# Kernel tuning notes

Hardware: AMD Instinct MI355X
Metric: run time of the kernel (lower is better)

Reference implementation:

```python
import jax, jax.numpy as jnp
import numpy as np

NUM_REGIONS = 20
EMBED_DIM = 768
PATCH = (4, 16, 16)          # (pd, ph, pw)
IMG = (64, 512, 512)         # (D, H, W)
B = 2
N_PATCHES = 16384


def setup_inputs() -> dict:
    key = jax.random.key(0)
    k1, k2, k3 = jax.random.split(key, 3)
    segmentation_mask = jax.random.randint(
        k1, (B, 1) + IMG, 0, NUM_REGIONS + 1, dtype=jnp.int32)
    patch_coords = jax.random.uniform(k2, (B, N_PATCHES, 3), dtype=jnp.float32)
    region_prototypes = 0.02 * jax.random.normal(
        k3, (NUM_REGIONS, EMBED_DIM), dtype=jnp.float32)
    return {"segmentation_mask": segmentation_mask,
            "patch_coords": patch_coords,
            "region_prototypes": region_prototypes}


def _compute_assignments(segmentation_mask, patch_coords):
    Bsz, _, D, H, W = segmentation_mask.shape
    pd, ph, pw = PATCH
    dims = jnp.array([D, H, W], dtype=jnp.float32)
    half = jnp.array([pd // 2, ph // 2, pw // 2], dtype=jnp.float32)

    cpix = patch_coords * dims                                   # (B,N,3)
    # torch: z_start = max(0, int(c - half)); z_end = min(D, int(c + half))
    start = jnp.maximum(0.0, jnp.floor(cpix - half)).astype(jnp.int32)   # (B,N,3)
    end = jnp.minimum(dims, jnp.floor(cpix + half)).astype(jnp.int32)    # (B,N,3)

    # per-axis index grids of fixed size, validity mask honors clipped box
    zi = start[..., 0:1] + jnp.arange(pd, dtype=jnp.int32)        # (B,N,pd)
    yi = start[..., 1:2] + jnp.arange(ph, dtype=jnp.int32)        # (B,N,ph)
    xi = start[..., 2:3] + jnp.arange(pw, dtype=jnp.int32)        # (B,N,pw)
    vz = zi < end[..., 0:1]
    vy = yi < end[..., 1:2]
    vx = xi < end[..., 2:3]

    ziC = jnp.clip(zi, 0, D - 1)
    yiC = jnp.clip(yi, 0, H - 1)
    xiC = jnp.clip(xi, 0, W - 1)

    # flattened gather: (B, N, pd, ph, pw) voxel values
    lin = (ziC[:, :, :, None, None] * (H * W)
           + yiC[:, :, None, :, None] * W
           + xiC[:, :, None, None, :])
    flat = segmentation_mask.reshape(Bsz, D * H * W)
    vals = jnp.take_along_axis(flat, lin.reshape(Bsz, -1), axis=1)
    vals = vals.reshape(Bsz, lin.shape[1], pd, ph, pw)
    valid = (vz[:, :, :, None, None]
             & vy[:, :, None, :, None]
             & vx[:, :, None, None, :])

    # numel of each (possibly clipped) crop
    extents = jnp.maximum(end - start, 0)                         # (B,N,3)
    numel = jnp.prod(extents, axis=-1).astype(jnp.float32)        # (B,N)

    # per-region counts; small fixed loop over 20 regions keeps memory low
    counts = jnp.stack(
        [jnp.sum((vals == r) & valid, axis=(2, 3, 4)).astype(jnp.float32)
         for r in range(1, NUM_REGIONS + 1)], axis=-1)            # (B,N,R)

    prop = counts / jnp.maximum(numel, 1.0)[..., None]            # zero crops -> 0
    a = prop + 1e-6
    a = a / jnp.sum(a, axis=-1, keepdims=True)
    return a


def reference(segmentation_mask, patch_coords, region_prototypes):
    Bsz = segmentation_mask.shape[0]
    region_features = jnp.broadcast_to(
        region_prototypes[None], (Bsz,) + region_prototypes.shape)
    patch_to_region = _compute_assignments(segmentation_mask, patch_coords)
    return region_features, patch_to_region
```

## Files before the change

### kernel.cpp

```cpp
#include <hip/hip_runtime.h>
#include <stdint.h>

#define NREG   20
#define EDIM   768
#define DVOL   64
#define HVOL   512
#define WVOL   512
#define HW_    (HVOL * WVOL)
#define DHW_   (DVOL * HVOL * WVOL)
#define NPATCH 16384
#define BTOT   2
#define PROTO_N (NREG * EDIM)
#define RF_N    (BTOT * PROTO_N)
#define TOTAL_PATCHES (BTOT * NPATCH)
#define NBUCKET 1024

#define W_COUNTS 0
#define W_OFFS   1024
#define W_KEYS   2048
#define W_PID    (W_KEYS + TOTAL_PATCHES)
#define W_C0     (W_PID  + TOTAL_PATCHES)
#define W_C1     (W_C0   + TOTAL_PATCHES)
#define W_C2     (W_C1   + TOTAL_PATCHES)

struct __attribute__((packed, aligned(4))) int4p { int x, y, z, w; };

__global__ __launch_bounds__(256) void count_kernel(
    const float* __restrict__ coords,
    const float* __restrict__ proto,
    float*       __restrict__ out,
    unsigned*    __restrict__ ws)
{
    const int p = (int)blockIdx.x * 256 + (int)threadIdx.x;

    if (p < RF_N) out[p] = proto[p >= PROTO_N ? p - PROTO_N : p];

    const int b = p >> 14;
    const float zf = coords[p * 3 + 0] * 64.0f;
    const float yf = coords[p * 3 + 1] * 512.0f;
    const int zbin = ((int)zf) >> 1;
    const int ybin = ((int)yf) >> 5;
    const unsigned key = (unsigned)(b * 512 + zbin * 16 + ybin);
    ws[W_KEYS + p] = key;
    atomicAdd(&ws[W_COUNTS + key], 1u);
}

__global__ __launch_bounds__(1024) void scan_kernel(unsigned* __restrict__ ws)
{
    __shared__ unsigned tmp[NBUCKET];
    const int t = threadIdx.x;
    const unsigned v = ws[W_COUNTS + t];
    tmp[t] = v;
    __syncthreads();
#pragma unroll
    for (int off = 1; off < NBUCKET; off <<= 1) {
        const unsigned y = (t >= off) ? tmp[t - off] : 0u;
        __syncthreads();
        tmp[t] += y;
        __syncthreads();
    }
    ws[W_OFFS + t] = tmp[t] - v;
}

__global__ __launch_bounds__(256) void scatter_kernel(
    const float* __restrict__ coords, unsigned* __restrict__ ws)
{
    const int p = (int)blockIdx.x * 256 + (int)threadIdx.x;
    const unsigned key  = ws[W_KEYS + p];
    const unsigned rank = atomicAdd(&ws[W_OFFS + key], 1u);
    ws[W_PID + rank] = (unsigned)p;
    ((float*)ws)[W_C0 + rank] = coords[p * 3 + 0];
    ((float*)ws)[W_C1 + rank] = coords[p * 3 + 1];
    ((float*)ws)[W_C2 + rank] = coords[p * 3 + 2];
}

__global__ __launch_bounds__(256) void assign_kernel(
    const int*      __restrict__ seg,
    const unsigned* __restrict__ ws,
    float*          __restrict__ out)
{
    const int bid  = (int)blockIdx.x;
    const int sbid = (bid & 7) * 1024 + (bid >> 3);

    const int lane = threadIdx.x & 63;
    const int wave = threadIdx.x >> 6;
    const int slot = sbid * 4 + wave;

    const int   patch = (int)ws[W_PID + slot];
    const float c0 = ((const float*)ws)[W_C0 + slot] * 64.0f;
    const float c1 = ((const float*)ws)[W_C1 + slot] * 512.0f;
    const float c2 = ((const float*)ws)[W_C2 + slot] * 512.0f;
    const int b = patch >> 14;

    const int sz = (int)fmaxf(0.0f,   floorf(c0 - 2.0f));
    const int ez = (int)fminf(64.0f,  floorf(c0 + 2.0f));
    const int sy = (int)fmaxf(0.0f,   floorf(c1 - 8.0f));
    const int ey = (int)fminf(512.0f, floorf(c1 + 8.0f));
    const int sx = (int)fmaxf(0.0f,   floorf(c2 - 8.0f));
    const int ex = (int)fminf(512.0f, floorf(c2 + 8.0f));

    const int xl4  = lane & 3;
    const int yy   = lane >> 2;
    const int p_lo = sx + 4 * xl4;
    const int st   = min(p_lo, WVOL - 4);
    const int yi   = sy + yy;
    const unsigned vy = (yi < ey) ? 0xFFFFFFFFu : 0u;
    const int yiC  = min(yi, HVOL - 1);
    const int rowbase = b * DHW_ + yiC * WVOL + st;

    unsigned vm[4];
#pragma unroll
    for (int j = 0; j < 4; ++j) {
        const int pos = st + j;
        vm[j] = (pos >= p_lo && pos < ex) ? vy : 0u;
    }

    int4p q0, q1, q2, q3;
    {
        const int z0 = min(sz + 0, DVOL - 1) * HW_;
        const int z1 = min(sz + 1, DVOL - 1) * HW_;
        const int z2 = min(sz + 2, DVOL - 1) * HW_;
        const int z3 = min(sz + 3, DVOL - 1) * HW_;
        q0 = *(const int4p*)(seg + rowbase + z0);
        q1 = *(const int4p*)(seg + rowbase + z1);
        q2 = *(const int4p*)(seg + rowbase + z2);
        q3 = *(const int4p*)(seg + rowbase + z3);
    }

    unsigned cc[5] = {0u, 0u, 0u, 0u, 0u};
#pragma unroll
    for (int z = 0; z < 4; ++z) {
        const unsigned zm = (sz + z < ez) ? 0xFFFFFFFFu : 0u;
        const int4p qz = (z == 0) ? q0 : (z == 1) ? q1 : (z == 2) ? q2 : q3;
        const int vals[4] = {qz.x, qz.y, qz.z, qz.w};
#pragma unroll
        for (int j = 0; j < 4; ++j) {
            const int v = vals[j] & (int)(vm[j] & zm);
            const int t = v - 1;
            const unsigned inc = 1u << ((t & 3) << 3);
            const int qk = t >> 2;
#pragma unroll
            for (int k = 0; k < 5; ++k)
                cc[k] += (qk == k) ? inc : 0u;
        }
    }

#pragma unroll
    for (int off = 1; off < 8; off <<= 1) {
#pragma unroll
        for (int k = 0; k < 5; ++k)
            cc[k] += (unsigned)__shfl_xor((int)cc[k], off);
    }

    unsigned lo[5], hi[5];
#pragma unroll
    for (int k = 0; k < 5; ++k) {
        lo[k] = cc[k] & 0x00FF00FFu;
        hi[k] = (cc[k] >> 8) & 0x00FF00FFu;
    }
#pragma unroll
    for (int off = 8; off < 64; off <<= 1) {
#pragma unroll
        for (int k = 0; k < 5; ++k) {
            lo[k] += (unsigned)__shfl_xor((int)lo[k], off);
            hi[k] += (unsigned)__shfl_xor((int)hi[k], off);
        }
    }

    unsigned S = 0u;
#pragma unroll
    for (int k = 0; k < 5; ++k) S += lo[k] + hi[k];
    const unsigned tot = (S & 0xFFFFu) + (S >> 16);

    const int r = lane & 3;
    const unsigned sLo = (lane < 4) ? lo[0] : (lane < 8) ? lo[1]
                       : (lane < 12) ? lo[2] : (lane < 16) ? lo[3] : lo[4];
    const unsigned sHi = (lane < 4) ? hi[0] : (lane < 8) ? hi[1]
                       : (lane < 12) ? hi[2] : (lane < 16) ? hi[3] : hi[4];
    const unsigned fld = (r & 1) ? sHi : sLo;
    const unsigned cnt = (r & 2) ? (fld >> 16) : (fld & 0xFFFFu);

    if (lane < NREG) {
        const float nz = (float)max(ez - sz, 0);
        const float ny = (float)max(ey - sy, 0);
        const float nx = (float)max(ex - sx, 0);
        const float denom = fmaxf(nz * ny * nx, 1.0f);
        const float s = (float)tot / denom + (float)NREG * 1e-6f;
        const float a = (float)cnt / denom + 1e-6f;
        out[RF_N + patch * NREG + lane] = a / s;
    }
}

extern "C" void kernel_launch(void* const* d_in, const int* in_sizes, int n_in,
                              void* d_out, int out_size, void* d_ws, size_t ws_size,
                              hipStream_t stream)
{
    const int*   seg    = (const int*)d_in[0];
    const float* coords = (const float*)d_in[1];
    const float* proto  = (const float*)d_in[2];
    float*       out    = (float*)d_out;
    unsigned*    ws     = (unsigned*)d_ws;

    hipMemsetAsync(ws, 0, NBUCKET * sizeof(unsigned), stream);
    hipLaunchKernelGGL(count_kernel, dim3(TOTAL_PATCHES / 256), dim3(256),
                       0, stream, coords, proto, out, ws);
    hipLaunchKernelGGL(scan_kernel, dim3(1), dim3(NBUCKET), 0, stream, ws);
    hipLaunchKernelGGL(scatter_kernel, dim3(TOTAL_PATCHES / 256), dim3(256),
                       0, stream, coords, ws);
    hipLaunchKernelGGL(assign_kernel, dim3(TOTAL_PATCHES / 4), dim3(256),
                       0, stream, seg, ws, out);
}
```

Baseline: 55.32 us.

## Fuse count, scan and scatter into one grid-synced sort kernel

Replaces the three-kernel bucket sort (global atomic count, single-block scan, atomic scatter) with one 8-block kernel. Each block counts its keys in shared memory, publishes per-block histograms, waits on a global atomic barrier, then computes its own offsets and scatters with shared-memory atomics. The prototype broadcast copy moves into the assign kernel. This is meant to remove two kernel launches and the global atomic contention, at the cost of a spin-wait barrier that relies on all 8 blocks being resident at once and of low parallelism in the sort phase.

```diff
diff --git a/kernel.cpp b/kernel.cpp
--- a/kernel.cpp
+++ b/kernel.cpp
@@ -14,71 +14,107 @@
 #define RF_N    (BTOT * PROTO_N)
 #define TOTAL_PATCHES (BTOT * NPATCH)
 #define NBUCKET 1024
-
-#define W_COUNTS 0
-#define W_OFFS   1024
-#define W_KEYS   2048
-#define W_PID    (W_KEYS + TOTAL_PATCHES)
-#define W_C0     (W_PID  + TOTAL_PATCHES)
-#define W_C1     (W_C0   + TOTAL_PATCHES)
-#define W_C2     (W_C1   + TOTAL_PATCHES)
+#define SORT_BLOCKS 8
+
+#define W_PHASE 0
+#define W_BCNT  32
+#define W_PID   (W_BCNT + SORT_BLOCKS * NBUCKET)
+#define W_C0    (W_PID  + TOTAL_PATCHES)
+#define W_C1    (W_C0   + TOTAL_PATCHES)
+#define W_C2    (W_C1   + TOTAL_PATCHES)
+#define MEMSET_WORDS (W_BCNT + SORT_BLOCKS * NBUCKET)
 
 struct __attribute__((packed, aligned(4))) int4p { int x, y, z, w; };
 
-__global__ __launch_bounds__(256) void count_kernel(
-    const float* __restrict__ coords,
-    const float* __restrict__ proto,
-    float*       __restrict__ out,
-    unsigned*    __restrict__ ws)
-{
-    const int p = (int)blockIdx.x * 256 + (int)threadIdx.x;
-
-    if (p < RF_N) out[p] = proto[p >= PROTO_N ? p - PROTO_N : p];
-
-    const int b = p >> 14;
-    const float zf = coords[p * 3 + 0] * 64.0f;
-    const float yf = coords[p * 3 + 1] * 512.0f;
-    const int zbin = ((int)zf) >> 1;
-    const int ybin = ((int)yf) >> 5;
-    const unsigned key = (unsigned)(b * 512 + zbin * 16 + ybin);
-    ws[W_KEYS + p] = key;
-    atomicAdd(&ws[W_COUNTS + key], 1u);
-}
-
-__global__ __launch_bounds__(1024) void scan_kernel(unsigned* __restrict__ ws)
-{
-    __shared__ unsigned tmp[NBUCKET];
-    const int t = threadIdx.x;
-    const unsigned v = ws[W_COUNTS + t];
-    tmp[t] = v;
-    __syncthreads();
-#pragma unroll
-    for (int off = 1; off < NBUCKET; off <<= 1) {
-        const unsigned y = (t >= off) ? tmp[t - off] : 0u;
-        __syncthreads();
-        tmp[t] += y;
-        __syncthreads();
-    }
-    ws[W_OFFS + t] = tmp[t] - v;
-}
-
-__global__ __launch_bounds__(256) void scatter_kernel(
+__global__ __launch_bounds__(1024) void sort_kernel(
     const float* __restrict__ coords, unsigned* __restrict__ ws)
 {
-    const int p = (int)blockIdx.x * 256 + (int)threadIdx.x;
-    const unsigned key  = ws[W_KEYS + p];
-    const unsigned rank = atomicAdd(&ws[W_OFFS + key], 1u);
-    ws[W_PID + rank] = (unsigned)p;
-    ((float*)ws)[W_C0 + rank] = coords[p * 3 + 0];
-    ((float*)ws)[W_C1 + rank] = coords[p * 3 + 1];
-    ((float*)ws)[W_C2 + rank] = coords[p * 3 + 2];
+    __shared__ unsigned lcnt[NBUCKET];
+    __shared__ unsigned lofs[NBUCKET];
+
+    float* wsf = (float*)ws;
+    const int blk = (int)blockIdx.x;
+    const int t   = (int)threadIdx.x;
+    const int p0  = blk * 4096 + t * 4;
+    const int b   = blk >> 2;
+
+    lcnt[t] = 0u;
+    __syncthreads();
+
+    float c[12];
+    {
+        const float4* cp = (const float4*)(coords + (size_t)p0 * 3);
+        const float4 a = cp[0], bb = cp[1], d = cp[2];
+        c[0]=a.x;  c[1]=a.y;  c[2]=a.z;  c[3]=a.w;  c[4]=bb.x; c[5]=bb.y;
+        c[6]=bb.z; c[7]=bb.w; c[8]=d.x;  c[9]=d.y;  c[10]=d.z; c[11]=d.w;
+    }
+    unsigned key[4];
+#pragma unroll
+    for (int i = 0; i < 4; ++i) {
+        const int zbin = ((int)(c[3*i + 0] * 64.0f))  >> 1;
+        const int ybin = ((int)(c[3*i + 1] * 512.0f)) >> 5;
+        key[i] = (unsigned)(b * 512 + zbin * 16 + ybin);
+        atomicAdd(&lcnt[key[i]], 1u);
+    }
+    __syncthreads();
+
+    ws[W_BCNT + blk * NBUCKET + t] = lcnt[t];
+    __syncthreads();
+
+    if (t == 0) {
+        __hip_atomic_fetch_add(&ws[W_PHASE], 1u,
+                               __ATOMIC_RELEASE, __HIP_MEMORY_SCOPE_AGENT);
+        int guard = 0;
+        while (__hip_atomic_load(&ws[W_PHASE],
+                 __ATOMIC_ACQUIRE, __HIP_MEMORY_SCOPE_AGENT) < SORT_BLOCKS
+               && guard < (1 << 22)) {
+            __builtin_amdgcn_s_sleep(1);
+            ++guard;
+        }
+    }
+    __syncthreads();
+
+    unsigned tot = 0u, before = 0u;
+#pragma unroll
+    for (int k = 0; k < SORT_BLOCKS; ++k) {
+        const unsigned v = ws[W_BCNT + k * NBUCKET + t];
+        tot += v;
+        before += (k < blk) ? v : 0u;
+    }
+    lcnt[t] = tot;
+    __syncthreads();
+
+#pragma unroll
+    for (int off = 1; off < NBUCKET; off <<= 1) {
+        const unsigned u = (t >= off) ? lcnt[t - off] : 0u;
+        __syncthreads();
+        lcnt[t] += u;
+        __syncthreads();
+    }
+    lofs[t] = (lcnt[t] - tot) + before;
+    __syncthreads();
+
+#pragma unroll
+    for (int i = 0; i < 4; ++i) {
+        const unsigned rank = atomicAdd(&lofs[key[i]], 1u);
+        ws[W_PID + rank] = (unsigned)(p0 + i);
+        wsf[W_C0 + rank] = c[3*i + 0];
+        wsf[W_C1 + rank] = c[3*i + 1];
+        wsf[W_C2 + rank] = c[3*i + 2];
+    }
 }
 
 __global__ __launch_bounds__(256) void assign_kernel(
     const int*      __restrict__ seg,
     const unsigned* __restrict__ ws,
+    const float*    __restrict__ proto,
     float*          __restrict__ out)
 {
+    if (blockIdx.x < RF_N / 256) {
+        const int i = (int)blockIdx.x * 256 + (int)threadIdx.x;
+        out[i] = proto[i >= PROTO_N ? i - PROTO_N : i];
+    }
+
     const int bid  = (int)blockIdx.x;
     const int sbid = (bid & 7) * 1024 + (bid >> 3);
 
@@ -201,12 +237,9 @@
     float*       out    = (float*)d_out;
     unsigned*    ws     = (unsigned*)d_ws;
 
-    hipMemsetAsync(ws, 0, NBUCKET * sizeof(unsigned), stream);
-    hipLaunchKernelGGL(count_kernel, dim3(TOTAL_PATCHES / 256), dim3(256),
-                       0, stream, coords, proto, out, ws);
-    hipLaunchKernelGGL(scan_kernel, dim3(1), dim3(NBUCKET), 0, stream, ws);
-    hipLaunchKernelGGL(scatter_kernel, dim3(TOTAL_PATCHES / 256), dim3(256),
+    hipMemsetAsync(ws, 0, MEMSET_WORDS * sizeof(unsigned), stream);
+    hipLaunchKernelGGL(sort_kernel, dim3(SORT_BLOCKS), dim3(1024),
                        0, stream, coords, ws);
     hipLaunchKernelGGL(assign_kernel, dim3(TOTAL_PATCHES / 4), dim3(256),
-                       0, stream, seg, ws, out);
+                       0, stream, seg, ws, proto, out);
 }
```

Result: faster. 52.60 us (-4.9%).
